# Kernel optimization log

Measured on AMD Instinct MI355X. Metric: run time of the kernel, lower is better.

Reference implementation:

```python
import jax, jax.numpy as jnp
import numpy as np

NUM_EMBEDDINGS = 1024
EMBEDDING_DIM = 64
BETA = 0.25
N_TOKENS = 131072


def setup_inputs() -> dict:
    key = jax.random.key(0)
    k_z, k_cb = jax.random.split(key)
    z = jax.random.normal(k_z, (N_TOKENS, EMBEDDING_DIM), dtype=jnp.float32)
    # nn.Embedding weight initialized uniform(-1/K, 1/K)
    codebook = jax.random.uniform(
        k_cb, (NUM_EMBEDDINGS, EMBEDDING_DIM), dtype=jnp.float32,
        minval=-1.0 / NUM_EMBEDDINGS, maxval=1.0 / NUM_EMBEDDINGS)
    return {"z": z, "codebook": codebook}


def reference(z, codebook):
    # z: [N, D], codebook: [K, D]
    z_flat = z.reshape(-1, z.shape[-1])
    # squared euclidean distances: ||z||^2 - 2 z.E^T + ||E||^2 -> [N, K]
    distances = (jnp.sum(z_flat * z_flat, axis=1, keepdims=True)
                 - 2.0 * jnp.einsum('nd,kd->nk', z_flat, codebook)
                 + jnp.sum(codebook * codebook, axis=1))
    indices = jnp.argmin(distances, axis=1)          # [N]
    z_q = codebook[indices].reshape(z.shape)          # [N, D]
    # commitment + codebook losses
    loss = (BETA * jnp.mean((jax.lax.stop_gradient(z_q) - z) ** 2)
            + jnp.mean((z_q - jax.lax.stop_gradient(z)) ** 2))
    # straight-through estimator
    z_q_st = z + jax.lax.stop_gradient(z_q - z)
    return z_q_st, loss
```

## Files before the change

kernel.cpp:

```cpp
#include <hip/hip_runtime.h>


typedef __attribute__((ext_vector_type(8))) short bf16x8;
typedef __attribute__((ext_vector_type(4))) float f32x4;

#define N_TOKENS 131072
#define DIM 64
#define DYN_LDS 135168

__device__ __forceinline__ short f32_bf16(float f) {
  unsigned u = __builtin_bit_cast(unsigned, f);
  unsigned r = u + 0x7FFFu + ((u >> 16) & 1u);
  return (short)(r >> 16);
}

__global__ __launch_bounds__(256) void vq_prep(
    const float* __restrict__ cb, unsigned short* __restrict__ ch,
    float* __restrict__ ca2) {
  const int lane = threadIdx.x & 63;
  const int wv = threadIdx.x >> 6;
  const int code = blockIdx.x * 4 + wv;
  const float e = cb[code * DIM + lane] * 1024.0f;
  ch[code * DIM + lane] = (unsigned short)f32_bf16(e);
  float sq = e * e;
  #pragma unroll
  for (int w = 32; w >= 1; w >>= 1) sq += __shfl_xor(sq, w, 64);
  if (lane == 0) ca2[code] = 128.0f - sq * (1.0f / 2048.0f);
}

__global__ __attribute__((amdgpu_flat_work_group_size(512, 512),
                          amdgpu_waves_per_eu(2, 2)))
void vq_argmin(
    const float* __restrict__ z, const unsigned short* __restrict__ ch,
    const float* __restrict__ ca2, const float* __restrict__ cb,
    float* __restrict__ out, double* __restrict__ part) {
  extern __shared__ char lds[];
  unsigned short* Bs = (unsigned short*)lds;
  float* ca_s = (float*)(lds + 131072);
  __shared__ float sml[8];

  const int tid = threadIdx.x, lane = tid & 63, wv = tid >> 6;
  const int g = lane >> 4, c15 = lane & 15, sw = c15 & 7;
  const size_t wrow = (size_t)blockIdx.x * 512 + (size_t)wv * 64;
  const unsigned kmask = 0xFFFFFC00u;

  #pragma unroll
  for (int q = 0; q < 16; ++q) {
    const int chunk = q * 512 + tid;
    const int code = chunk >> 3, c = chunk & 7;
    __builtin_amdgcn_global_load_lds(
        (const __attribute__((address_space(1))) unsigned int*)
            (ch + code * DIM + ((c ^ (code & 7)) << 3)),
        (__attribute__((address_space(3))) unsigned int*)(Bs + chunk * 8),
        16, 0, 0);
  }
  if (tid < 256)
    __builtin_amdgcn_global_load_lds(
        (const __attribute__((address_space(1))) unsigned int*)(ca2 + tid * 4),
        (__attribute__((address_space(3))) unsigned int*)(ca_s + tid * 4),
        16, 0, 0);

  f32x4 a0[2][2][2];
  const float* zb = z + wrow * DIM;
  #pragma unroll
  for (int m = 0; m < 2; ++m)
    #pragma unroll
    for (int kk = 0; kk < 2; ++kk) {
      const float* p = zb + (m * 16 + c15) * DIM + kk * 32 + g * 8;
      a0[m][kk][0] = *(const f32x4*)p;
      a0[m][kk][1] = *(const f32x4*)(p + 4);
    }

  __syncthreads();

  f32x4 a1[2][2][2];
  #pragma unroll
  for (int m = 0; m < 2; ++m)
    #pragma unroll
    for (int kk = 0; kk < 2; ++kk) {
      const float* p = zb + ((m + 2) * 16 + c15) * DIM + kk * 32 + g * 8;
      a1[m][kk][0] = *(const f32x4*)p;
      a1[m][kk][1] = *(const f32x4*)(p + 4);
    }

  bf16x8 ah[4][2];
  float zsq = 0.0f;
  #pragma unroll
  for (int m = 0; m < 2; ++m)
    #pragma unroll
    for (int kk = 0; kk < 2; ++kk)
      #pragma unroll
      for (int j = 0; j < 4; ++j) {
        const float v0 = a0[m][kk][0][j], v1 = a0[m][kk][1][j];
        ah[m][kk][j]     = f32_bf16(v0);
        ah[m][kk][j + 4] = f32_bf16(v1);
        zsq += v0 * v0 + v1 * v1;
      }
  #pragma unroll
  for (int m = 0; m < 2; ++m)
    #pragma unroll
    for (int kk = 0; kk < 2; ++kk)
      #pragma unroll
      for (int j = 0; j < 4; ++j) {
        const float v0 = a1[m][kk][0][j], v1 = a1[m][kk][1][j];
        ah[m + 2][kk][j]     = f32_bf16(v0);
        ah[m + 2][kk][j + 4] = f32_bf16(v1);
        zsq += v0 * v0 + v1 * v1;
      }

  unsigned best[4][4];
  #pragma unroll
  for (int m = 0; m < 4; ++m)
    #pragma unroll
    for (int r = 0; r < 4; ++r) best[m][r] = 0u;

  const char* bsp = (const char*)Bs;
  const int bx0 = (g ^ sw) << 4;
  const int bx1 = ((4 + g) ^ sw) << 4;

  auto LDB = [&](int t, bf16x8& b00, bf16x8& b01, bf16x8& b10, bf16x8& b11,
                 float& cA, float& cB) {
    const int r0 = (t * 32 + c15) * 128;
    b00 = *(const bf16x8*)(bsp + r0 + bx0);
    b01 = *(const bf16x8*)(bsp + r0 + bx1);
    b10 = *(const bf16x8*)(bsp + r0 + 2048 + bx0);
    b11 = *(const bf16x8*)(bsp + r0 + 2048 + bx1);
    cA = ca_s[t * 32 + c15];
    cB = ca_s[t * 32 + 16 + c15];
  };
  auto MM = [&](int t, bf16x8 b00, bf16x8 b01, bf16x8 b10, bf16x8 b11,
                float cA, float cB) {
    f32x4 acc[2][4];
    __builtin_amdgcn_s_setprio(1);
    #pragma unroll
    for (int n = 0; n < 2; ++n) {
      const bf16x8 f0 = n ? b10 : b00;
      const bf16x8 f1 = n ? b11 : b01;
      const float can = n ? cB : cA;
      const f32x4 cv = {can, can, can, can};
      #pragma unroll
      for (int m = 0; m < 4; ++m) {
        acc[n][m] = __builtin_amdgcn_mfma_f32_16x16x32_bf16(
            ah[m][0], f0, cv, 0, 0, 0);
        acc[n][m] = __builtin_amdgcn_mfma_f32_16x16x32_bf16(
            ah[m][1], f1, acc[n][m], 0, 0, 0);
      }
    }
    __builtin_amdgcn_s_setprio(0);
    #pragma unroll
    for (int n = 0; n < 2; ++n) {
      const unsigned cc = 1023u - (unsigned)(t * 32 + n * 16 + c15);
      #pragma unroll
      for (int m = 0; m < 4; ++m)
        #pragma unroll
        for (int r = 0; r < 4; ++r) {
          const unsigned key =
              (__builtin_bit_cast(unsigned, acc[n][m][r]) & kmask) | cc;
          best[m][r] = key > best[m][r] ? key : best[m][r];
        }
    }
  };

  bf16x8 x00, x01, x10, x11, y00, y01, y10, y11;
  float cx0, cx1, cy0, cy1;
  LDB(0, x00, x01, x10, x11, cx0, cx1);
  #pragma unroll 1
  for (int t2 = 0; t2 < 16; ++t2) {
    LDB(t2 * 2 + 1, y00, y01, y10, y11, cy0, cy1);
    MM(t2 * 2, x00, x01, x10, x11, cx0, cx1);
    LDB((t2 * 2 + 2) & 31, x00, x01, x10, x11, cx0, cx1);
    MM(t2 * 2 + 1, y00, y01, y10, y11, cy0, cy1);
  }

  float lossx = 0.0f;
  const f32x4* cb4 = (const f32x4*)cb;
  f32x4* out4 = (f32x4*)out;
  #pragma unroll
  for (int m = 0; m < 4; ++m)
    #pragma unroll
    for (int r = 0; r < 4; ++r) {
      unsigned bk = best[m][r];
      #pragma unroll
      for (int w = 1; w < 16; w <<= 1) {
        const unsigned ob = (unsigned)__shfl_xor((int)bk, w, 64);
        bk = ob > bk ? ob : bk;
      }
      const int row = m * 16 + g * 4 + r;
      const int bi = 1023 - (int)(bk & 1023u);
      out4[(wrow + row) * 16 + c15] = cb4[bi * 16 + c15];
      if (c15 == 0) lossx += 128.0f - __builtin_bit_cast(float, bk & kmask);
    }

  float psum = zsq + lossx * (1.0f / 512.0f);
  #pragma unroll
  for (int w = 32; w >= 1; w >>= 1) psum += __shfl_xor(psum, w, 64);
  if (lane == 0) sml[wv] = psum;
  __syncthreads();
  if (tid == 0) {
    double t = 0.0;
    #pragma unroll
    for (int i = 0; i < 8; ++i) t += (double)sml[i];
    part[blockIdx.x] = t;
  }
}

__global__ __launch_bounds__(256) void vq_finalize(
    const double* __restrict__ part, float* __restrict__ out_loss) {
  __shared__ double s[4];
  const int tid = threadIdx.x, lane = tid & 63, wv = tid >> 6;
  double v = part[tid];
  #pragma unroll
  for (int w = 32; w >= 1; w >>= 1) v += __shfl_xor(v, w, 64);
  if (lane == 0) s[wv] = v;
  __syncthreads();
  if (tid == 0)
    out_loss[0] = (float)(1.25 * (s[0] + s[1] + s[2] + s[3]) /
                          ((double)N_TOKENS * (double)DIM));
}

extern "C" void kernel_launch(void* const* d_in, const int* in_sizes, int n_in,
                              void* d_out, int out_size, void* d_ws, size_t ws_size,
                              hipStream_t stream) {
  const float* z = (const float*)d_in[0];
  const float* cb = (const float*)d_in[1];
  float* out = (float*)d_out;
  char* ws = (char*)d_ws;

  unsigned short* ch = (unsigned short*)(ws);
  float* ca2 = (float*)(ws + 131072);
  double* part = (double*)(ws + 135168);

  (void)hipFuncSetAttribute((const void*)vq_argmin,
                            hipFuncAttributeMaxDynamicSharedMemorySize, DYN_LDS);

  vq_prep<<<256, 256, 0, stream>>>(cb, ch, ca2);
  vq_argmin<<<256, 512, DYN_LDS, stream>>>(z, ch, ca2, cb, out, part);
  vq_finalize<<<1, 256, 0, stream>>>(part, out + (size_t)N_TOKENS * DIM);
}
```

Measured before the change: 33.79 us.

## Switch distance GEMM to FP8 MFMA and fuse loss finalize via last-block atomic

Converts the codebook and z tiles to FP8 (e4m3) and uses 16x16x32 fp8 MFMA instead of bf16, halving the codebook LDS footprint and LDS read traffic. Blocks shrink to 256 threads with 512 blocks to fit more workgroups per CU. The separate finalize kernel is replaced by a last-block-done atomic counter reduction, with a memset to reset the counter. FP8 quantization risks argmin mismatches when candidate distances are close, since the reduced precision may change which code is selected.

```diff
diff --git a/kernel.cpp b/kernel.cpp
--- a/kernel.cpp
+++ b/kernel.cpp
@@ -1,64 +1,65 @@
 #include <hip/hip_runtime.h>
 
 
-typedef __attribute__((ext_vector_type(8))) short bf16x8;
 typedef __attribute__((ext_vector_type(4))) float f32x4;
+typedef __attribute__((ext_vector_type(2))) long long llx2;
 
 #define N_TOKENS 131072
 #define DIM 64
-#define DYN_LDS 135168
-
-__device__ __forceinline__ short f32_bf16(float f) {
-  unsigned u = __builtin_bit_cast(unsigned, f);
-  unsigned r = u + 0x7FFFu + ((u >> 16) & 1u);
-  return (short)(r >> 16);
+#define DYN_LDS 69632
+
+__global__ __launch_bounds__(256) void vq_prep8(
+    const float* __restrict__ cb, unsigned* __restrict__ ch8,
+    float* __restrict__ ca2) {
+  const int t = threadIdx.x;
+  const int code = blockIdx.x * 16 + (t >> 4);
+  const int l = t & 15;
+  const int k0 = ((l >> 1) & 1) * 32 + (l >> 2) * 8 + (l & 1) * 4;
+  const f32x4 v = *(const f32x4*)(cb + code * DIM + k0);
+  const float e0 = v[0] * 1024.0f, e1 = v[1] * 1024.0f;
+  const float e2 = v[2] * 1024.0f, e3 = v[3] * 1024.0f;
+  unsigned p = __builtin_amdgcn_cvt_pk_fp8_f32(e0, e1, 0, false);
+  p = __builtin_amdgcn_cvt_pk_fp8_f32(e2, e3, p, true);
+  ch8[code * 16 + l] = p;
+  float sq = e0 * e0 + e1 * e1 + e2 * e2 + e3 * e3;
+  #pragma unroll
+  for (int w = 1; w < 16; w <<= 1) sq += __shfl_xor(sq, w, 64);
+  if (l == 0) ca2[code] = 128.0f - sq * (1.0f / 2048.0f);
 }
 
-__global__ __launch_bounds__(256) void vq_prep(
-    const float* __restrict__ cb, unsigned short* __restrict__ ch,
-    float* __restrict__ ca2) {
-  const int lane = threadIdx.x & 63;
-  const int wv = threadIdx.x >> 6;
-  const int code = blockIdx.x * 4 + wv;
-  const float e = cb[code * DIM + lane] * 1024.0f;
-  ch[code * DIM + lane] = (unsigned short)f32_bf16(e);
-  float sq = e * e;
-  #pragma unroll
-  for (int w = 32; w >= 1; w >>= 1) sq += __shfl_xor(sq, w, 64);
-  if (lane == 0) ca2[code] = 128.0f - sq * (1.0f / 2048.0f);
-}
-
-__global__ __attribute__((amdgpu_flat_work_group_size(512, 512),
+__global__ __attribute__((amdgpu_flat_work_group_size(256, 256),
                           amdgpu_waves_per_eu(2, 2)))
 void vq_argmin(
-    const float* __restrict__ z, const unsigned short* __restrict__ ch,
+    const float* __restrict__ z, const unsigned* __restrict__ ch8,
     const float* __restrict__ ca2, const float* __restrict__ cb,
-    float* __restrict__ out, double* __restrict__ part) {
+    float* __restrict__ out, double* __restrict__ part,
+    unsigned* __restrict__ cnt) {
   extern __shared__ char lds[];
-  unsigned short* Bs = (unsigned short*)lds;
-  float* ca_s = (float*)(lds + 131072);
-  __shared__ float sml[8];
+  unsigned* B8 = (unsigned*)lds;
+  float* ca_s = (float*)(lds + 65536);
+  __shared__ float sml[4];
+  __shared__ int lastflag;
+  __shared__ double swav[4];
 
   const int tid = threadIdx.x, lane = tid & 63, wv = tid >> 6;
-  const int g = lane >> 4, c15 = lane & 15, sw = c15 & 7;
-  const size_t wrow = (size_t)blockIdx.x * 512 + (size_t)wv * 64;
+  const int g = lane >> 4, c15 = lane & 15;
+  const size_t wrow = (size_t)blockIdx.x * 256 + (size_t)wv * 64;
   const unsigned kmask = 0xFFFFFC00u;
 
   #pragma unroll
   for (int q = 0; q < 16; ++q) {
-    const int chunk = q * 512 + tid;
-    const int code = chunk >> 3, c = chunk & 7;
+    const int chunk = q * 256 + tid;
+    const int code = chunk >> 2, c2 = chunk & 3;
     __builtin_amdgcn_global_load_lds(
         (const __attribute__((address_space(1))) unsigned int*)
-            (ch + code * DIM + ((c ^ (code & 7)) << 3)),
-        (__attribute__((address_space(3))) unsigned int*)(Bs + chunk * 8),
+            (ch8 + code * 16 + ((c2 ^ (code & 3)) << 2)),
+        (__attribute__((address_space(3))) unsigned int*)(B8 + chunk * 4),
         16, 0, 0);
   }
-  if (tid < 256)
-    __builtin_amdgcn_global_load_lds(
-        (const __attribute__((address_space(1))) unsigned int*)(ca2 + tid * 4),
-        (__attribute__((address_space(3))) unsigned int*)(ca_s + tid * 4),
-        16, 0, 0);
+  __builtin_amdgcn_global_load_lds(
+      (const __attribute__((address_space(1))) unsigned int*)(ca2 + tid * 4),
+      (__attribute__((address_space(3))) unsigned int*)(ca_s + tid * 4),
+      16, 0, 0);
 
   f32x4 a0[2][2][2];
   const float* zb = z + wrow * DIM;
@@ -83,30 +84,36 @@
       a1[m][kk][1] = *(const f32x4*)(p + 4);
     }
 
-  bf16x8 ah[4][2];
   float zsq = 0.0f;
-  #pragma unroll
-  for (int m = 0; m < 2; ++m)
-    #pragma unroll
-    for (int kk = 0; kk < 2; ++kk)
-      #pragma unroll
-      for (int j = 0; j < 4; ++j) {
-        const float v0 = a0[m][kk][0][j], v1 = a0[m][kk][1][j];
-        ah[m][kk][j]     = f32_bf16(v0);
-        ah[m][kk][j + 4] = f32_bf16(v1);
-        zsq += v0 * v0 + v1 * v1;
-      }
-  #pragma unroll
-  for (int m = 0; m < 2; ++m)
-    #pragma unroll
-    for (int kk = 0; kk < 2; ++kk)
-      #pragma unroll
-      for (int j = 0; j < 4; ++j) {
-        const float v0 = a1[m][kk][0][j], v1 = a1[m][kk][1][j];
-        ah[m + 2][kk][j]     = f32_bf16(v0);
-        ah[m + 2][kk][j + 4] = f32_bf16(v1);
-        zsq += v0 * v0 + v1 * v1;
-      }
+  auto pack8 = [&](const f32x4& v0, const f32x4& v1) -> long long {
+    unsigned lo = __builtin_amdgcn_cvt_pk_fp8_f32(v0[0], v0[1], 0, false);
+    lo = __builtin_amdgcn_cvt_pk_fp8_f32(v0[2], v0[3], lo, true);
+    unsigned hi = __builtin_amdgcn_cvt_pk_fp8_f32(v1[0], v1[1], 0, false);
+    hi = __builtin_amdgcn_cvt_pk_fp8_f32(v1[2], v1[3], hi, true);
+    return (long long)(((unsigned long long)hi << 32) | (unsigned long long)lo);
+  };
+
+  long long ah[4][2];
+  #pragma unroll
+  for (int m = 0; m < 2; ++m)
+    #pragma unroll
+    for (int kk = 0; kk < 2; ++kk) {
+      ah[m][kk] = pack8(a0[m][kk][0], a0[m][kk][1]);
+      #pragma unroll
+      for (int j = 0; j < 4; ++j)
+        zsq += a0[m][kk][0][j] * a0[m][kk][0][j]
+             + a0[m][kk][1][j] * a0[m][kk][1][j];
+    }
+  #pragma unroll
+  for (int m = 0; m < 2; ++m)
+    #pragma unroll
+    for (int kk = 0; kk < 2; ++kk) {
+      ah[m + 2][kk] = pack8(a1[m][kk][0], a1[m][kk][1]);
+      #pragma unroll
+      for (int j = 0; j < 4; ++j)
+        zsq += a1[m][kk][0][j] * a1[m][kk][0][j]
+             + a1[m][kk][1][j] * a1[m][kk][1][j];
+    }
 
   unsigned best[4][4];
   #pragma unroll
@@ -114,36 +121,30 @@
     #pragma unroll
     for (int r = 0; r < 4; ++r) best[m][r] = 0u;
 
-  const char* bsp = (const char*)Bs;
-  const int bx0 = (g ^ sw) << 4;
-  const int bx1 = ((4 + g) ^ sw) << 4;
-
-  auto LDB = [&](int t, bf16x8& b00, bf16x8& b01, bf16x8& b10, bf16x8& b11,
-                 float& cA, float& cB) {
-    const int r0 = (t * 32 + c15) * 128;
-    b00 = *(const bf16x8*)(bsp + r0 + bx0);
-    b01 = *(const bf16x8*)(bsp + r0 + bx1);
-    b10 = *(const bf16x8*)(bsp + r0 + 2048 + bx0);
-    b11 = *(const bf16x8*)(bsp + r0 + 2048 + bx1);
+  const char* bsp = (const char*)B8;
+  const int slot = (g ^ (c15 & 3)) << 4;
+
+  auto LDB = [&](int t, llx2& b0, llx2& b1, float& cA, float& cB) {
+    const int r0 = (t * 32 + c15) * 64;
+    b0 = *(const llx2*)(bsp + r0 + slot);
+    b1 = *(const llx2*)(bsp + r0 + 1024 + slot);
     cA = ca_s[t * 32 + c15];
     cB = ca_s[t * 32 + 16 + c15];
   };
-  auto MM = [&](int t, bf16x8 b00, bf16x8 b01, bf16x8 b10, bf16x8 b11,
-                float cA, float cB) {
+  auto MM = [&](int t, llx2 b0, llx2 b1, float cA, float cB) {
     f32x4 acc[2][4];
     __builtin_amdgcn_s_setprio(1);
     #pragma unroll
     for (int n = 0; n < 2; ++n) {
-      const bf16x8 f0 = n ? b10 : b00;
-      const bf16x8 f1 = n ? b11 : b01;
+      const llx2 f = n ? b1 : b0;
       const float can = n ? cB : cA;
       const f32x4 cv = {can, can, can, can};
       #pragma unroll
       for (int m = 0; m < 4; ++m) {
-        acc[n][m] = __builtin_amdgcn_mfma_f32_16x16x32_bf16(
-            ah[m][0], f0, cv, 0, 0, 0);
-        acc[n][m] = __builtin_amdgcn_mfma_f32_16x16x32_bf16(
-            ah[m][1], f1, acc[n][m], 0, 0, 0);
+        acc[n][m] = __builtin_amdgcn_mfma_f32_16x16x32_fp8_fp8(
+            ah[m][0], f[0], cv, 0, 0, 0);
+        acc[n][m] = __builtin_amdgcn_mfma_f32_16x16x32_fp8_fp8(
+            ah[m][1], f[1], acc[n][m], 0, 0, 0);
       }
     }
     __builtin_amdgcn_s_setprio(0);
@@ -161,15 +162,15 @@
     }
   };
 
-  bf16x8 x00, x01, x10, x11, y00, y01, y10, y11;
+  llx2 x0, x1, y0, y1;
   float cx0, cx1, cy0, cy1;
-  LDB(0, x00, x01, x10, x11, cx0, cx1);
+  LDB(0, x0, x1, cx0, cx1);
   #pragma unroll 1
   for (int t2 = 0; t2 < 16; ++t2) {
-    LDB(t2 * 2 + 1, y00, y01, y10, y11, cy0, cy1);
-    MM(t2 * 2, x00, x01, x10, x11, cx0, cx1);
-    LDB((t2 * 2 + 2) & 31, x00, x01, x10, x11, cx0, cx1);
-    MM(t2 * 2 + 1, y00, y01, y10, y11, cy0, cy1);
+    LDB(t2 * 2 + 1, y0, y1, cy0, cy1);
+    MM(t2 * 2, x0, x1, cx0, cx1);
+    LDB((t2 * 2 + 2) & 31, x0, x1, cx0, cx1);
+    MM(t2 * 2 + 1, y0, y1, cy0, cy1);
   }
 
   float lossx = 0.0f;
@@ -197,25 +198,30 @@
   if (lane == 0) sml[wv] = psum;
   __syncthreads();
   if (tid == 0) {
-    double t = 0.0;
-    #pragma unroll
-    for (int i = 0; i < 8; ++i) t += (double)sml[i];
-    part[blockIdx.x] = t;
-  }
-}
-
-__global__ __launch_bounds__(256) void vq_finalize(
-    const double* __restrict__ part, float* __restrict__ out_loss) {
-  __shared__ double s[4];
-  const int tid = threadIdx.x, lane = tid & 63, wv = tid >> 6;
-  double v = part[tid];
-  #pragma unroll
-  for (int w = 32; w >= 1; w >>= 1) v += __shfl_xor(v, w, 64);
-  if (lane == 0) s[wv] = v;
+    const double t = (double)sml[0] + (double)sml[1]
+                   + (double)sml[2] + (double)sml[3];
+    __hip_atomic_store(&part[blockIdx.x], t, __ATOMIC_RELEASE,
+                       __HIP_MEMORY_SCOPE_AGENT);
+    const unsigned old = __hip_atomic_fetch_add(cnt, 1u, __ATOMIC_ACQ_REL,
+                                                __HIP_MEMORY_SCOPE_AGENT);
+    lastflag = (old == 511u);
+  }
   __syncthreads();
-  if (tid == 0)
-    out_loss[0] = (float)(1.25 * (s[0] + s[1] + s[2] + s[3]) /
-                          ((double)N_TOKENS * (double)DIM));
+
+  if (lastflag) {
+    double v = __hip_atomic_load(&part[tid], __ATOMIC_ACQUIRE,
+                                 __HIP_MEMORY_SCOPE_AGENT)
+             + __hip_atomic_load(&part[tid + 256], __ATOMIC_ACQUIRE,
+                                 __HIP_MEMORY_SCOPE_AGENT);
+    #pragma unroll
+    for (int w = 32; w >= 1; w >>= 1) v += __shfl_xor(v, w, 64);
+    if (lane == 0) swav[wv] = v;
+    __syncthreads();
+    if (tid == 0)
+      out[(size_t)N_TOKENS * DIM] =
+          (float)(1.25 * (swav[0] + swav[1] + swav[2] + swav[3]) /
+                  ((double)N_TOKENS * (double)DIM));
+  }
 }
 
 extern "C" void kernel_launch(void* const* d_in, const int* in_sizes, int n_in,
@@ -226,14 +232,15 @@
   float* out = (float*)d_out;
   char* ws = (char*)d_ws;
 
-  unsigned short* ch = (unsigned short*)(ws);
-  float* ca2 = (float*)(ws + 131072);
-  double* part = (double*)(ws + 135168);
+  unsigned* ch8 = (unsigned*)(ws);
+  float* ca2 = (float*)(ws + 65536);
+  unsigned* cnt = (unsigned*)(ws + 69632);
+  double* part = (double*)(ws + 69640);
 
   (void)hipFuncSetAttribute((const void*)vq_argmin,
                             hipFuncAttributeMaxDynamicSharedMemorySize, DYN_LDS);
 
-  vq_prep<<<256, 256, 0, stream>>>(cb, ch, ca2);
-  vq_argmin<<<256, 512, DYN_LDS, stream>>>(z, ch, ca2, cb, out, part);
-  vq_finalize<<<1, 256, 0, stream>>>(part, out + (size_t)N_TOKENS * DIM);
+  hipMemsetAsync(cnt, 0, sizeof(unsigned), stream);
+  vq_prep8<<<64, 256, 0, stream>>>(cb, ch8, ca2);
+  vq_argmin<<<512, 256, DYN_LDS, stream>>>(z, ch8, ca2, cb, out, part, cnt);
 }
```

New measurement: 67.70 us. 2x slower.
